# Kernel optimization log

Hardware: AMD Instinct MI355X
Metric: run time of the kernel (lower is better)

The kernel has to match this reference:

```python
import jax, jax.numpy as jnp
import numpy as np

N_NODES = 300000
N_EDGES = 1200000
D = 128
B = 1000
VOCAB = 26  # vocab_size + 1


def setup_inputs() -> dict:
    key = jax.random.key(0)
    ks = jax.random.split(key, 10)
    x = jax.random.randint(ks[0], (N_NODES,), 0, VOCAB, dtype=jnp.int32)
    edge_index = jax.random.randint(ks[1], (2, N_EDGES), 0, N_NODES, dtype=jnp.int32)
    # cumulative protein boundaries: B proteins of equal length, last entry == N_NODES
    amino_acids_numbers = (jnp.arange(1, B + 1, dtype=jnp.int32) * (N_NODES // B))
    s = 1.0 / np.sqrt(D)
    emb = jax.random.normal(ks[2], (VOCAB, D), dtype=jnp.float32)
    W_rel1 = jax.random.uniform(ks[3], (D, D), jnp.float32, -s, s)
    b_rel1 = jax.random.uniform(ks[4], (D,), jnp.float32, -s, s)
    W_root1 = jax.random.uniform(ks[5], (D, D), jnp.float32, -s, s)
    W_rel2 = jax.random.uniform(ks[6], (D, D), jnp.float32, -s, s)
    b_rel2 = jax.random.uniform(ks[7], (D,), jnp.float32, -s, s)
    W_root2 = jax.random.uniform(ks[8], (D, D), jnp.float32, -s, s)
    return {"x": x, "edge_index": edge_index, "amino_acids_numbers": amino_acids_numbers,
            "emb": emb, "W_rel1": W_rel1, "b_rel1": b_rel1, "W_root1": W_root1,
            "W_rel2": W_rel2, "b_rel2": b_rel2, "W_root2": W_root2}


def _graph_conv(nodes, src, tgt, W_rel, b_rel, W_root, n):
    # PyG GraphConv (aggr='add'): out = Lin_rel(sum_{j->i} x_j) + Lin_root(x_i)
    agg = jax.ops.segment_sum(nodes[src], tgt, num_segments=n)  # [N, D]
    return agg @ W_rel.T + b_rel + nodes @ W_root.T


def reference(x, edge_index, amino_acids_numbers, emb,
              W_rel1, b_rel1, W_root1, W_rel2, b_rel2, W_root2):
    n = x.shape[0]
    src, tgt = edge_index[0], edge_index[1]
    nodes = emb[x]  # [N, D] embedding lookup
    nodes = _graph_conv(nodes, src, tgt, W_rel1, b_rel1, W_root1, n)
    nodes = _graph_conv(nodes, src, tgt, W_rel2, b_rel2, W_root2, n)
    # segment mean pooling over [start:end) slices defined by cumulative ends
    ends = amino_acids_numbers
    seg = jnp.searchsorted(ends, jnp.arange(n), side='right')  # node -> protein id
    b = ends.shape[0]
    sums = jax.ops.segment_sum(nodes, seg, num_segments=b)  # [B, D]
    counts = jnp.diff(ends, prepend=jnp.zeros((1,), ends.dtype)).astype(nodes.dtype)
    return sums / counts[:, None]
```

## Files before the change

kernel.cpp:

```cpp
#include <hip/hip_runtime.h>

#define DD 128
#define VV 26
#define NW 13
#define CS4 4
#define G 256
#define TWIN 512
#define PAD 4096
#define SBITS 19

__device__ __forceinline__ unsigned wsum(unsigned v) {
#pragma unroll
    for (int m = 32; m >= 1; m >>= 1) v += __shfl_xor(v, m, 64);
    return v;
}

__device__ __forceinline__ int wscan_incl(int v) {
    int lane = threadIdx.x & 63;
#pragma unroll
    for (int off = 1; off < 64; off <<= 1) {
        int t = __shfl_up(v, off, 64);
        if (lane >= off) v += t;
    }
    return v;
}

__device__ __forceinline__ int seg_guess(const int* ends, int B, int t, int Lavg) {
    int p = t / Lavg;
    if (p > B - 1) p = B - 1;
    while (p > 0 && ends[p - 1] > t) --p;
    while (ends[p] <= t) ++p;
    return p;
}

__device__ __forceinline__ int bseg(const int* cumx, int j) {
    int lo = 0, hi = G - 1;
    while (lo < hi) {
        int mid = (lo + hi + 1) >> 1;
        if (cumx[mid] <= j) lo = mid; else hi = mid - 1;
    }
    return lo;
}

__global__ __launch_bounds__(1024)
void k_sort_pre(const int* __restrict__ src, const int* __restrict__ tgt,
                const int* __restrict__ ends,
                int E, int B, int chunk, int Lavg,
                const float* __restrict__ emb,
                const float* __restrict__ W1r, const float* __restrict__ b1,
                const float* __restrict__ W1o,
                const float* __restrict__ W2r, const float* __restrict__ W2o,
                unsigned* __restrict__ sorted_ts,
                int* __restrict__ segstartT, int* __restrict__ seghistT,
                float* __restrict__ P1, float* __restrict__ P2,
                float* __restrict__ P3, float* __restrict__ uvec,
                float* __restrict__ wvec) {
    extern __shared__ char smem[];
    int tid = threadIdx.x;
    int chunkp = (chunk + 1) & ~1;

    if (blockIdx.x >= G) {
        float* e1r = (float*)smem;
        float* r1r = e1r + DD;
        float* b1s = r1r + DD;
        int v = blockIdx.x - G;
        int d = tid;
        if (d < DD) {
            const float* e = emb + v * DD;
            const float* w1r = W1r + d * DD;
            const float* w1o = W1o + d * DD;
            float s1 = 0.f, s2 = 0.f;
            for (int k = 0; k < DD; ++k) { float ev = e[k]; s1 += ev * w1r[k]; s2 += ev * w1o[k]; }
            e1r[d] = s1; r1r[d] = s2; b1s[d] = b1[d];
        }
        __syncthreads();
        if (d < DD) {
            const float* wr = W2r + d * DD;
            const float* wo = W2o + d * DD;
            float p1 = 0.f, p2 = 0.f, p3 = 0.f, su = 0.f, sw = 0.f;
            for (int k = 0; k < DD; ++k) {
                float a = wr[k], bb = wo[k], ee = e1r[k], r = r1r[k], c = b1s[k];
                p1 += ee * a; p2 += r * a + ee * bb; p3 += r * bb;
                su += c * a; sw += c * bb;
            }
            P1[v * DD + d] = p1; P2[v * DD + d] = p2; P3[v * DD + d] = p3;
            if (v == 0) { uvec[d] = su; wvec[d] = sw; }
        }
        return;
    }

    unsigned* pay = (unsigned*)smem;
    int* lds_ends = (int*)(pay + chunk);
    int* hist = lds_ends + 1024;
    int* cur = hist + 1024;
    int* wsums = cur + 1024;
    unsigned short* lpe = (unsigned short*)(wsums + 16);

    int b = blockIdx.x;
    int e0 = b * chunk;
    int e1 = min(E, e0 + chunk);
    int clen = e1 - e0;

    for (int i = tid; i < B; i += 1024) lds_ends[i] = ends[i];
    hist[tid] = 0;
    __syncthreads();

    for (int i = tid; i < clen; i += 1024) {
        int t = tgt[e0 + i];
        int p = seg_guess(lds_ends, B, t, Lavg);
        atomicAdd(&hist[p], 1);
        lpe[i] = (unsigned short)p;
    }
    __syncthreads();

    int v = hist[tid];
    if (tid < B) seghistT[tid * G + b] = v;
    int wave = tid >> 6, lane = tid & 63;
    int incl = wscan_incl(v);
    if (lane == 63) wsums[wave] = incl;
    __syncthreads();
    int offw = 0;
    for (int w = 0; w < wave; ++w) offw += wsums[w];
    int excl = incl + offw - v;
    if (tid < B) {
        cur[tid] = excl;
        segstartT[tid * G + b] = e0 + excl;
    }
    __syncthreads();

    for (int i = tid; i < clen; i += 1024) {
        int e = e0 + i;
        int p = lpe[i];
        int s = src[e];
        int t = tgt[e];
        int pst = (p == 0) ? 0 : lds_ends[p - 1];
        int pos = atomicAdd(&cur[p], 1);
        pay[pos] = ((unsigned)(t - pst) << SBITS) | (unsigned)s;
    }
    __syncthreads();

    for (int i = tid; i < clen; i += 1024) sorted_ts[e0 + i] = pay[i];
}

__global__ __launch_bounds__(256)
void k_counts(const int* __restrict__ x, const int* __restrict__ ends,
              const int* __restrict__ seghistT, const int* __restrict__ segstartT,
              int B, int E, const unsigned* __restrict__ sorted_ts,
              unsigned* __restrict__ counts, unsigned* __restrict__ csG,
              int* __restrict__ DpG, float* __restrict__ CpG) {
    __shared__ unsigned tab[TWIN * CS4];
    __shared__ int cumx[G + 4], segb[G], wsums[4];
    __shared__ unsigned red[4][16];
    int p = blockIdx.x, tid = threadIdx.x;
    int wave = tid >> 6, lane = tid & 63;
    int start = (p == 0) ? 0 : ends[p - 1];
    int end = ends[p];
    int Lp = end - start;

    int h = seghistT[p * G + tid];
    segb[tid] = segstartT[p * G + tid];
    int incl = wscan_incl(h);
    if (lane == 63) wsums[wave] = incl;
    __syncthreads();
    int offw = 0;
    for (int w = 0; w < wave; ++w) offw += wsums[w];
    cumx[tid] = incl + offw - h;
    if (tid == 255) { cumx[G] = incl + offw; DpG[p] = incl + offw; }
    __syncthreads();
    int Dp = cumx[G];

    unsigned cp[16];
#pragma unroll
    for (int k = 0; k < 16; ++k) cp[k] = 0u;

    for (int w0 = 0; w0 < Lp; w0 += TWIN) {
        int wlen = min(TWIN, Lp - w0);
        __syncthreads();
        for (int i = tid; i < wlen * CS4; i += 256) tab[i] = 0u;
        __syncthreads();
        for (int j = tid; j < Dp; j += 256) {
            int bb = bseg(cumx, j);
            int pos = segb[bb] + (j - cumx[bb]);
            unsigned ts = sorted_ts[pos];
            int s = (int)(ts & ((1u << SBITS) - 1u));
            int tloc = (int)(ts >> SBITS) - w0;
            if (w0 == 0) csG[(size_t)p * PAD + j] = (unsigned)s;
            if ((unsigned)tloc < (unsigned)wlen) {
                int lbl = x[s];
                atomicAdd(&tab[tloc * CS4 + (lbl >> 3)], 1u << ((lbl & 7) * 4));
            }
        }
        __syncthreads();
        unsigned* dst = counts + ((size_t)(start + w0)) * CS4;
        for (int i = tid; i < wlen * CS4; i += 256) dst[i] = tab[i];
        for (int r = tid; r < wlen; r += 256) {
            uint4 c0 = *reinterpret_cast<const uint4*>(&tab[r * CS4]);
            unsigned w;
            w = c0.x; cp[0]  += w & 0x000F000Fu; cp[1]  += (w >> 4) & 0x000F000Fu;
                      cp[2]  += (w >> 8) & 0x000F000Fu; cp[3]  += (w >> 12) & 0x000F000Fu;
            w = c0.y; cp[4]  += w & 0x000F000Fu; cp[5]  += (w >> 4) & 0x000F000Fu;
                      cp[6]  += (w >> 8) & 0x000F000Fu; cp[7]  += (w >> 12) & 0x000F000Fu;
            w = c0.z; cp[8]  += w & 0x000F000Fu; cp[9]  += (w >> 4) & 0x000F000Fu;
                      cp[10] += (w >> 8) & 0x000F000Fu; cp[11] += (w >> 12) & 0x000F000Fu;
            w = c0.w; cp[12] += w & 0x000F000Fu; cp[13] += (w >> 4) & 0x000F000Fu;
                      cp[14] += (w >> 8) & 0x000F000Fu; cp[15] += (w >> 12) & 0x000F000Fu;
        }
    }

#pragma unroll
    for (int k = 0; k < 16; ++k) {
        unsigned a = wsum(cp[k]); if (lane == 0) red[wave][k] = a;
    }
    __syncthreads();
    if (tid < 16) {
        unsigned t = red[0][tid] + red[1][tid] + red[2][tid] + red[3][tid];
        int base = 8 * (tid >> 2) + (tid & 3);
        if (base < VV) CpG[(size_t)p * VV + base] = (float)(t & 0xFFFFu);
        if (base + 4 < VV) CpG[(size_t)p * VV + base + 4] = (float)(t >> 16);
    }
}

__global__ __launch_bounds__(256)
void k_protein(const int* __restrict__ x, const int* __restrict__ ends,
               const int* __restrict__ DpG, const unsigned* __restrict__ csG,
               const unsigned* __restrict__ counts, const float* __restrict__ CpG,
               const float* __restrict__ P1, const float* __restrict__ P2,
               const float* __restrict__ P3, const float* __restrict__ uvec,
               const float* __restrict__ wvec, const float* __restrict__ b2,
               int B, int E, float* __restrict__ out) {
    __shared__ unsigned red[4][32];
    __shared__ float c2f[VV], cpf[VV], hpf[VV];
    int p = blockIdx.x, tid = threadIdx.x;
    int wave = tid >> 6, lane = tid & 63;
    int start = (p == 0) ? 0 : ends[p - 1];
    int end = ends[p];
    int Dp = DpG[p];

    if (tid < VV) cpf[tid] = CpG[(size_t)p * VV + tid];

    unsigned c2[16], hpw[NW];
#pragma unroll
    for (int k = 0; k < 16; ++k) c2[k] = 0u;
#pragma unroll
    for (int w = 0; w < NW; ++w) hpw[w] = 0u;

    const unsigned* cs = csG + (size_t)p * PAD;
    for (int j = tid; j < Dp; j += 256) {
        int s = (int)cs[j];
        uint4 c0 = *reinterpret_cast<const uint4*>(counts + (size_t)s * CS4);
        unsigned w;
        w = c0.x; c2[0]  += w & 0x000F000Fu; c2[1]  += (w >> 4) & 0x000F000Fu;
                  c2[2]  += (w >> 8) & 0x000F000Fu; c2[3]  += (w >> 12) & 0x000F000Fu;
        w = c0.y; c2[4]  += w & 0x000F000Fu; c2[5]  += (w >> 4) & 0x000F000Fu;
                  c2[6]  += (w >> 8) & 0x000F000Fu; c2[7]  += (w >> 12) & 0x000F000Fu;
        w = c0.z; c2[8]  += w & 0x000F000Fu; c2[9]  += (w >> 4) & 0x000F000Fu;
                  c2[10] += (w >> 8) & 0x000F000Fu; c2[11] += (w >> 12) & 0x000F000Fu;
        w = c0.w; c2[12] += w & 0x000F000Fu; c2[13] += (w >> 4) & 0x000F000Fu;
                  c2[14] += (w >> 8) & 0x000F000Fu; c2[15] += (w >> 12) & 0x000F000Fu;
    }

    for (int i = start + tid; i < end; i += 256) {
        int l = x[i];
        unsigned inc = 1u << ((l & 1) * 16);
        int wi = l >> 1;
#pragma unroll
        for (int w2 = 0; w2 < NW; ++w2) hpw[w2] += (w2 == wi) ? inc : 0u;
    }

#pragma unroll
    for (int k = 0; k < 16; ++k) {
        unsigned a = wsum(c2[k]); if (lane == 0) red[wave][k] = a;
    }
#pragma unroll
    for (int w = 0; w < NW; ++w) {
        unsigned a = wsum(hpw[w]); if (lane == 0) red[wave][16 + w] = a;
    }
    __syncthreads();
    if (tid < 16 + NW) {
        unsigned t = red[0][tid] + red[1][tid] + red[2][tid] + red[3][tid];
        if (tid < 16) {
            int base = 8 * (tid >> 2) + (tid & 3);
            if (base < VV) c2f[base] = (float)(t & 0xFFFFu);
            if (base + 4 < VV) c2f[base + 4] = (float)(t >> 16);
        } else {
            int w = tid - 16;
            hpf[w * 2] = (float)(t & 0xFFFFu);
            if (w * 2 + 1 < VV) hpf[w * 2 + 1] = (float)(t >> 16);
        }
    }
    __syncthreads();

    if (tid < DD) {
        int d = tid;
        float acc = 0.f;
#pragma unroll
        for (int v = 0; v < VV; ++v)
            acc += c2f[v] * P1[v * DD + d] + cpf[v] * P2[v * DD + d] + hpf[v] * P3[v * DD + d];
        float Lp = (float)(end - start);
        float invL = 1.f / Lp;
        float Dpf = (float)Dp;
        out[(size_t)p * DD + d] = acc * invL + (Dpf * invL) * uvec[d] + wvec[d] + b2[d];
    }
}

extern "C" void kernel_launch(void* const* d_in, const int* in_sizes, int n_in,
                              void* d_out, int out_size, void* d_ws, size_t ws_size,
                              hipStream_t stream) {
    const int*   x       = (const int*)d_in[0];
    const int*   edge    = (const int*)d_in[1];
    const int*   ends    = (const int*)d_in[2];
    const float* emb     = (const float*)d_in[3];
    const float* W_rel1  = (const float*)d_in[4];
    const float* b_rel1  = (const float*)d_in[5];
    const float* W_root1 = (const float*)d_in[6];
    const float* W_rel2  = (const float*)d_in[7];
    const float* b_rel2  = (const float*)d_in[8];
    const float* W_root2 = (const float*)d_in[9];

    const int N = in_sizes[0];
    const int E = in_sizes[1] / 2;
    const int B = in_sizes[2];
    const int Lavg = (N / B) > 0 ? (N / B) : 1;
    const int chunk = (E + G - 1) / G;
    const int chunkp = (chunk + 1) & ~1;

    const int* srcp = edge;
    const int* tgtp = edge + E;

    auto align256 = [](size_t v) { return (v + 255) & ~(size_t)255; };
    char* ws = (char*)d_ws;
    size_t off = 0;
    unsigned* counts = (unsigned*)(ws + off);                 off += align256((size_t)N * CS4 * 4);
    int* segstartT = (int*)(ws + off);                        off += align256((size_t)B * G * 4);
    int* seghistT = (int*)(ws + off);                         off += align256((size_t)B * G * 4);
    int* DpG = (int*)(ws + off);                              off += align256((size_t)B * 4);
    unsigned* sorted_ts = (unsigned*)(ws + off);              off += align256((size_t)E * 4);
    unsigned* csG = (unsigned*)(ws + off);                    off += align256((size_t)B * PAD * 4);
    float* CpG = (float*)(ws + off);                          off += align256((size_t)B * VV * 4);
    float* P1 = (float*)(ws + off);                           off += align256((size_t)VV * DD * 4);
    float* P2 = (float*)(ws + off);                           off += align256((size_t)VV * DD * 4);
    float* P3 = (float*)(ws + off);                           off += align256((size_t)VV * DD * 4);
    float* uvec = (float*)(ws + off);                         off += align256((size_t)DD * 4);
    float* wvec = (float*)(ws + off);                         off += align256((size_t)DD * 4);
    (void)ws_size; (void)n_in; (void)out_size;


    size_t ldsb = (size_t)chunk * 4 + (size_t)(3 * 1024 + 16) * 4 + (size_t)chunkp * 2;
    k_sort_pre<<<G + VV, 1024, ldsb, stream>>>(
        srcp, tgtp, ends, E, B, chunk, Lavg,
        emb, W_rel1, b_rel1, W_root1, W_rel2, W_root2,
        sorted_ts, segstartT, seghistT, P1, P2, P3, uvec, wvec);

    k_counts<<<B, 256, 0, stream>>>(x, ends, seghistT, segstartT, B, E, sorted_ts,
                                    counts, csG, DpG, CpG);

    k_protein<<<B, 256, 0, stream>>>(x, ends, DpG, csG, counts, CpG,
                                     P1, P2, P3, uvec, wvec, b_rel2, B, E, (float*)d_out);
}
```

Measured before the change: 60.27 us.

## Stage edge payloads in LDS and move per-protein label histogram into counts kernel

The sort kernel now reads src and tgt once in the histogram pass, packs the payload into an extra LDS buffer, and the scatter pass copies from LDS instead of re-reading global memory. The per-protein label histogram over x moves from k_protein into k_counts and is passed through a new HpG buffer, which shortens the protein kernel's critical path. In exchange, sort blocks need twice the LDS for payloads, which may lower occupancy, and k_counts does more work.

Measured after the change: 60.54 us. About the same (+0.4%).

```diff
diff --git a/kernel.cpp b/kernel.cpp
--- a/kernel.cpp
+++ b/kernel.cpp
@@ -89,7 +89,8 @@
         return;
     }
 
-    unsigned* pay = (unsigned*)smem;
+    unsigned* payL = (unsigned*)smem;
+    unsigned* pay = payL + chunk;
     int* lds_ends = (int*)(pay + chunk);
     int* hist = lds_ends + 1024;
     int* cur = hist + 1024;
@@ -107,9 +108,12 @@
 
     for (int i = tid; i < clen; i += 1024) {
         int t = tgt[e0 + i];
+        int s = src[e0 + i];
         int p = seg_guess(lds_ends, B, t, Lavg);
         atomicAdd(&hist[p], 1);
         lpe[i] = (unsigned short)p;
+        int pst = (p == 0) ? 0 : lds_ends[p - 1];
+        payL[i] = ((unsigned)(t - pst) << SBITS) | (unsigned)s;
     }
     __syncthreads();
 
@@ -129,13 +133,9 @@
     __syncthreads();
 
     for (int i = tid; i < clen; i += 1024) {
-        int e = e0 + i;
         int p = lpe[i];
-        int s = src[e];
-        int t = tgt[e];
-        int pst = (p == 0) ? 0 : lds_ends[p - 1];
         int pos = atomicAdd(&cur[p], 1);
-        pay[pos] = ((unsigned)(t - pst) << SBITS) | (unsigned)s;
+        pay[pos] = payL[i];
     }
     __syncthreads();
 
@@ -147,10 +147,11 @@
               const int* __restrict__ seghistT, const int* __restrict__ segstartT,
               int B, int E, const unsigned* __restrict__ sorted_ts,
               unsigned* __restrict__ counts, unsigned* __restrict__ csG,
-              int* __restrict__ DpG, float* __restrict__ CpG) {
+              int* __restrict__ DpG, float* __restrict__ CpG,
+              float* __restrict__ HpG) {
     __shared__ unsigned tab[TWIN * CS4];
     __shared__ int cumx[G + 4], segb[G], wsums[4];
-    __shared__ unsigned red[4][16];
+    __shared__ unsigned red[4][32];
     int p = blockIdx.x, tid = threadIdx.x;
     int wave = tid >> 6, lane = tid & 63;
     int start = (p == 0) ? 0 : ends[p - 1];
@@ -169,9 +170,19 @@
     __syncthreads();
     int Dp = cumx[G];
 
-    unsigned cp[16];
+    unsigned cp[16], hpw[NW];
 #pragma unroll
     for (int k = 0; k < 16; ++k) cp[k] = 0u;
+#pragma unroll
+    for (int w = 0; w < NW; ++w) hpw[w] = 0u;
+
+    for (int i = start + tid; i < end; i += 256) {
+        int l = x[i];
+        unsigned inc = 1u << ((l & 1) * 16);
+        int wi = l >> 1;
+#pragma unroll
+        for (int w2 = 0; w2 < NW; ++w2) hpw[w2] += (w2 == wi) ? inc : 0u;
+    }
 
     for (int w0 = 0; w0 < Lp; w0 += TWIN) {
         int wlen = min(TWIN, Lp - w0);
@@ -211,24 +222,35 @@
     for (int k = 0; k < 16; ++k) {
         unsigned a = wsum(cp[k]); if (lane == 0) red[wave][k] = a;
     }
-    __syncthreads();
-    if (tid < 16) {
+#pragma unroll
+    for (int w = 0; w < NW; ++w) {
+        unsigned a = wsum(hpw[w]); if (lane == 0) red[wave][16 + w] = a;
+    }
+    __syncthreads();
+    if (tid < 16 + NW) {
         unsigned t = red[0][tid] + red[1][tid] + red[2][tid] + red[3][tid];
-        int base = 8 * (tid >> 2) + (tid & 3);
-        if (base < VV) CpG[(size_t)p * VV + base] = (float)(t & 0xFFFFu);
-        if (base + 4 < VV) CpG[(size_t)p * VV + base + 4] = (float)(t >> 16);
+        if (tid < 16) {
+            int base = 8 * (tid >> 2) + (tid & 3);
+            if (base < VV) CpG[(size_t)p * VV + base] = (float)(t & 0xFFFFu);
+            if (base + 4 < VV) CpG[(size_t)p * VV + base + 4] = (float)(t >> 16);
+        } else {
+            int w = tid - 16;
+            HpG[(size_t)p * VV + w * 2] = (float)(t & 0xFFFFu);
+            if (w * 2 + 1 < VV) HpG[(size_t)p * VV + w * 2 + 1] = (float)(t >> 16);
+        }
     }
 }
 
 __global__ __launch_bounds__(256)
-void k_protein(const int* __restrict__ x, const int* __restrict__ ends,
+void k_protein(const int* __restrict__ ends,
                const int* __restrict__ DpG, const unsigned* __restrict__ csG,
                const unsigned* __restrict__ counts, const float* __restrict__ CpG,
+               const float* __restrict__ HpG,
                const float* __restrict__ P1, const float* __restrict__ P2,
                const float* __restrict__ P3, const float* __restrict__ uvec,
                const float* __restrict__ wvec, const float* __restrict__ b2,
                int B, int E, float* __restrict__ out) {
-    __shared__ unsigned red[4][32];
+    __shared__ unsigned red[4][16];
     __shared__ float c2f[VV], cpf[VV], hpf[VV];
     int p = blockIdx.x, tid = threadIdx.x;
     int wave = tid >> 6, lane = tid & 63;
@@ -237,12 +259,11 @@
     int Dp = DpG[p];
 
     if (tid < VV) cpf[tid] = CpG[(size_t)p * VV + tid];
-
-    unsigned c2[16], hpw[NW];
+    if (tid >= 32 && tid < 32 + VV) hpf[tid - 32] = HpG[(size_t)p * VV + (tid - 32)];
+
+    unsigned c2[16];
 #pragma unroll
     for (int k = 0; k < 16; ++k) c2[k] = 0u;
-#pragma unroll
-    for (int w = 0; w < NW; ++w) hpw[w] = 0u;
 
     const unsigned* cs = csG + (size_t)p * PAD;
     for (int j = tid; j < Dp; j += 256) {
@@ -259,34 +280,16 @@
                   c2[14] += (w >> 8) & 0x000F000Fu; c2[15] += (w >> 12) & 0x000F000Fu;
     }
 
-    for (int i = start + tid; i < end; i += 256) {
-        int l = x[i];
-        unsigned inc = 1u << ((l & 1) * 16);
-        int wi = l >> 1;
-#pragma unroll
-        for (int w2 = 0; w2 < NW; ++w2) hpw[w2] += (w2 == wi) ? inc : 0u;
-    }
-
 #pragma unroll
     for (int k = 0; k < 16; ++k) {
         unsigned a = wsum(c2[k]); if (lane == 0) red[wave][k] = a;
     }
-#pragma unroll
-    for (int w = 0; w < NW; ++w) {
-        unsigned a = wsum(hpw[w]); if (lane == 0) red[wave][16 + w] = a;
-    }
-    __syncthreads();
-    if (tid < 16 + NW) {
+    __syncthreads();
+    if (tid < 16) {
         unsigned t = red[0][tid] + red[1][tid] + red[2][tid] + red[3][tid];
-        if (tid < 16) {
-            int base = 8 * (tid >> 2) + (tid & 3);
-            if (base < VV) c2f[base] = (float)(t & 0xFFFFu);
-            if (base + 4 < VV) c2f[base + 4] = (float)(t >> 16);
-        } else {
-            int w = tid - 16;
-            hpf[w * 2] = (float)(t & 0xFFFFu);
-            if (w * 2 + 1 < VV) hpf[w * 2 + 1] = (float)(t >> 16);
-        }
+        int base = 8 * (tid >> 2) + (tid & 3);
+        if (base < VV) c2f[base] = (float)(t & 0xFFFFu);
+        if (base + 4 < VV) c2f[base + 4] = (float)(t >> 16);
     }
     __syncthreads();
 
@@ -337,6 +340,7 @@
     unsigned* sorted_ts = (unsigned*)(ws + off);              off += align256((size_t)E * 4);
     unsigned* csG = (unsigned*)(ws + off);                    off += align256((size_t)B * PAD * 4);
     float* CpG = (float*)(ws + off);                          off += align256((size_t)B * VV * 4);
+    float* HpG = (float*)(ws + off);                          off += align256((size_t)B * VV * 4);
     float* P1 = (float*)(ws + off);                           off += align256((size_t)VV * DD * 4);
     float* P2 = (float*)(ws + off);                           off += align256((size_t)VV * DD * 4);
     float* P3 = (float*)(ws + off);                           off += align256((size_t)VV * DD * 4);
@@ -345,15 +349,15 @@
     (void)ws_size; (void)n_in; (void)out_size;
 
 
-    size_t ldsb = (size_t)chunk * 4 + (size_t)(3 * 1024 + 16) * 4 + (size_t)chunkp * 2;
+    size_t ldsb = (size_t)chunk * 8 + (size_t)(3 * 1024 + 16) * 4 + (size_t)chunkp * 2;
     k_sort_pre<<<G + VV, 1024, ldsb, stream>>>(
         srcp, tgtp, ends, E, B, chunk, Lavg,
         emb, W_rel1, b_rel1, W_root1, W_rel2, W_root2,
         sorted_ts, segstartT, seghistT, P1, P2, P3, uvec, wvec);
 
     k_counts<<<B, 256, 0, stream>>>(x, ends, seghistT, segstartT, B, E, sorted_ts,
-                                    counts, csG, DpG, CpG);
-
-    k_protein<<<B, 256, 0, stream>>>(x, ends, DpG, csG, counts, CpG,
+                                    counts, csG, DpG, CpG, HpG);
+
+    k_protein<<<B, 256, 0, stream>>>(ends, DpG, csG, counts, CpG, HpG,
                                      P1, P2, P3, uvec, wvec, b_rel2, B, E, (float*)d_out);
 }
```
